# Performance work log

Measured on AMD Instinct MI355X. Metric: run time of the kernel, lower is better.

Reference implementation:

```python
import jax, jax.numpy as jnp
import numpy as np

B, T, IN_DIM, HID_DIM = 64, 1024, 256, 256


def setup_inputs() -> dict:
    key = jax.random.key(0)
    ks = jax.random.split(key, 5)
    glorot = np.sqrt(6.0 / (IN_DIM + HID_DIM * 2)).astype(np.float32)
    def W(k):
        return jax.random.uniform(k, (IN_DIM + HID_DIM, HID_DIM), jnp.float32, -glorot, glorot)
    return {
        "x": jax.random.normal(ks[0], (B, T, IN_DIM), jnp.float32),
        "W_i": W(ks[1]), "b_i": jnp.zeros((HID_DIM,), jnp.float32),
        "W_f": W(ks[2]), "b_f": jnp.zeros((HID_DIM,), jnp.float32),
        "W_o": W(ks[3]), "b_o": jnp.zeros((HID_DIM,), jnp.float32),
        "W_c": W(ks[4]), "b_c": jnp.zeros((HID_DIM,), jnp.float32),
    }


def reference(x, W_i, b_i, W_f, b_f, W_o, b_o, W_c, b_c):
    # x: [B, T, in_dim] -> time-major [T, B, in_dim]
    xt = jnp.transpose(x, (1, 0, 2))
    batch = x.shape[0]
    c0 = jnp.zeros((batch, HID_DIM), x.dtype)
    h0 = jnp.zeros((batch, HID_DIM), x.dtype)

    def step(carry, x_t):
        c, h = carry
        hx = jnp.concatenate([h, x_t], axis=1)  # [B, hid+in]
        i = jax.nn.sigmoid(hx @ W_i + b_i)
        f = jax.nn.sigmoid(hx @ W_f + b_f)
        o = jax.nn.sigmoid(hx @ W_o + b_o)
        c_new = f * c + i * jnp.tanh(hx @ W_c + b_c)
        h_new = o * jnp.tanh(c_new)
        return (c_new, h_new), h_new

    _, outputs = jax.lax.scan(step, (c0, h0), xt)
    return outputs  # [T, B, hid_dim]
```

## Files before the change

kernel.cpp:

```cpp
#include <hip/hip_runtime.h>
#include <hip/hip_fp16.h>
#include <cstdint>

typedef _Float16 f16x8 __attribute__((ext_vector_type(8)));
typedef float f32x4 __attribute__((ext_vector_type(4)));
typedef int i32x4 __attribute__((ext_vector_type(4)));


#define XG_OFF    0ULL
#define XG_BYTES  134217728ULL
#define AP_OFF    (XG_OFF + XG_BYTES)
#define AP_BYTES  33554432ULL
#define BP_OFF    (AP_OFF + AP_BYTES)
#define BP_BYTES  524288ULL
#define WAP_OFF   (BP_OFF + BP_BYTES)
#define WAP_BYTES 262144ULL
#define BIAS_OFF  (WAP_OFF + WAP_BYTES)

#define GLOROT 0.08838834764831845f
#define CSC    (GLOROT / 16129.0f)
#define CSCI   (-1.44269504f * CSC)
#define CSCC   (2.88539008f * CSC)
#define QINV   (127.0f / GLOROT)

#define EXP2(x) __builtin_amdgcn_exp2f(x)
#define RCP(x)  __builtin_amdgcn_rcpf(x)

__global__ void pack_weights(const float* __restrict__ Wi, const float* __restrict__ Wf,
                             const float* __restrict__ Wo, const float* __restrict__ Wc,
                             const float* __restrict__ bi, const float* __restrict__ bf,
                             const float* __restrict__ bo, const float* __restrict__ bc,
                             int8_t* __restrict__ WAp, __half* __restrict__ Bp,
                             float* __restrict__ bias_eff)
{
    int tidg = blockIdx.x * blockDim.x + threadIdx.x;
    if (tidg < 262144) {
        int i  = tidg & 15;
        int l  = (tidg >> 4) & 63;
        int kt = (tidg >> 10) & 3;
        int M  = tidg >> 12;
        int c  = 16 * M + (l & 15);
        int u  = c >> 2, gi = c & 3;
        int khi = kt * 4 + (l >> 4);
        int us  = 16 * khi + 4 * (i & 3) + (i >> 2);
        const float* W = (gi == 0) ? Wi : (gi == 1) ? Wf : (gi == 2) ? Wo : Wc;
        float q = rintf(W[us * 256 + u] * QINV);
        q = fminf(127.f, fmaxf(-127.f, q));
        WAp[tidg] = (int8_t)(int)q;
    } else if (tidg < 262144 + 262144) {
        int beta = tidg - 262144;
        int i = beta & 7;
        int l = (beta >> 3) & 63;
        int kk = (beta >> 9) & 7;
        int n = beta >> 12;
        int c = n * 16 + (l & 15);
        int u = c >> 2, g = c & 3;
        int k = kk * 32 + (l >> 4) * 8 + i;
        const float* W = (g == 0) ? Wi : (g == 1) ? Wf : (g == 2) ? Wo : Wc;
        Bp[beta] = __float2half(W[(256 + k) * 256 + u]);
    } else if (tidg < 262144 + 262144 + 1024) {
        int c = tidg - 524288;
        int g = c & 3;
        const float* bb = (g == 0) ? bi : (g == 1) ? bf : (g == 2) ? bo : bc;
        bias_eff[c] = bb[c >> 2];
    }
}

__global__ void pack_a(const float* __restrict__ x, __half* __restrict__ Ap)
{
    int t = blockIdx.x * blockDim.x + threadIdx.x;
    int l  = t & 63;
    int kk = (t >> 6) & 7;
    int m  = t >> 9;
    int row = m * 16 + (l & 15);
    int k0  = kk * 32 + (l >> 4) * 8;
    const float* src = x + (size_t)row * 256 + k0;
    f16x8 v;
#pragma unroll
    for (int i = 0; i < 8; ++i) v[i] = (_Float16)src[i];
    *reinterpret_cast<f16x8*>(Ap + (size_t)t * 8) = v;
}

__global__ __launch_bounds__(256) void gemm_xg(const __half* __restrict__ Ap,
                                               const __half* __restrict__ Bp,
                                               const float* __restrict__ bias_eff,
                                               __half* __restrict__ xgh)
{
    int wave = threadIdx.x >> 6;
    int lane = threadIdx.x & 63;
    int mtile = blockIdx.x * 4 + wave;
    int ntbase = blockIdx.y * 16;

    f16x8 a[8];
#pragma unroll
    for (int kk = 0; kk < 8; ++kk)
        a[kk] = *reinterpret_cast<const f16x8*>(Ap + ((size_t)(mtile * 8 + kk) * 64 + lane) * 8);

    int col_lo = lane & 15;
    int rgrp = lane >> 4;
#pragma unroll 1
    for (int j = 0; j < 16; ++j) {
        int nt = ntbase + j;
        int c = nt * 16 + col_lo;
        float bb = bias_eff[c];
        f32x4 acc = {bb, bb, bb, bb};
#pragma unroll
        for (int kk = 0; kk < 8; ++kk) {
            f16x8 bfr = *reinterpret_cast<const f16x8*>(Bp + ((size_t)(nt * 8 + kk) * 64 + lane) * 8);
            acc = __builtin_amdgcn_mfma_f32_16x16x32_f16(a[kk], bfr, acc, 0, 0, 0);
        }
        int u = c >> 2, gi = c & 3;
        float gsc = (gi == 3) ? 2.88539008f : -1.44269504f;
        int M2 = u >> 2, rga = u & 3;
        int wv = M2 >> 2, mt = M2 & 3;
#pragma unroll
        for (int r2 = 0; r2 < 4; ++r2) {
            int row = mtile * 16 + rgrp * 4 + r2;
            int b = row >> 10, t = row & 1023;
            int gW = b >> 4, bl = b & 15;
            size_t idx = ((((size_t)(t * 4 + gW) * 16 + wv) * 64 + (rga * 16 + bl)) * 4 + mt) * 4 + gi;
            xgh[idx] = __float2half(acc[r2] * gsc);
        }
    }
}

#define WKL(F) F(0,0) F(0,1) F(0,2) F(0,3) F(1,0) F(1,1) F(1,2) F(1,3) \
  F(2,0) F(2,1) F(2,2) F(2,3) F(3,0) F(3,1) F(3,2) F(3,3)

__global__ __launch_bounds__(1024, 4) void lstm_rec(
    const int8_t* __restrict__ WAp,
    const __half* __restrict__ xgp,
    float* __restrict__ out)
{
    const int g = blockIdx.x;
    const int tid = threadIdx.x;
    const int w = tid >> 6;
    const int l = tid & 63;
    const int bl = l & 15;
    const int rg = l >> 4;

    __shared__ int8_t HB[2][4096];

    const i32x4* wap = reinterpret_cast<const i32x4*>(WAp);
#define DECLW(mt, kt) i32x4 wq_##mt##_##kt = wap[(((4 * w + (mt)) * 4 + (kt)) * 64) + l];
    WKL(DECLW)
#undef DECLW

    int ra[4];
#pragma unroll
    for (int kt = 0; kt < 4; ++kt)
        ra[kt] = bl * 256 + ((((kt * 4) + rg) ^ bl) & 15) * 16;
    const int wab = bl * 256 + ((w ^ bl) & 15) * 16 + rg * 4;

    i32x4 b0 = {0, 0, 0, 0}, b1 = b0, b2 = b0, b3 = b0;
    float cs_0 = 0.f, cs_1 = 0.f, cs_2 = 0.f, cs_3 = 0.f;

    const __half* xp = xgp + ((size_t)(g * 16 + w) * 64 + l) * 16;
    f16x8 xA0 = *reinterpret_cast<const f16x8*>(xp);
    f16x8 xA1 = *reinterpret_cast<const f16x8*>(xp + 8);
    f16x8 xB0, xB1;

    float* op = out + (size_t)(16 * g + bl) * 256 + 16 * w + rg;

#define DOMT(mt, XH) { \
        i32x4 acc = {0, 0, 0, 0}; \
        acc = __builtin_amdgcn_mfma_i32_16x16x64_i8(wq_##mt##_0, b0, acc, 0, 0, 0); \
        acc = __builtin_amdgcn_mfma_i32_16x16x64_i8(wq_##mt##_1, b1, acc, 0, 0, 0); \
        acc = __builtin_amdgcn_mfma_i32_16x16x64_i8(wq_##mt##_2, b2, acc, 0, 0, 0); \
        acc = __builtin_amdgcn_mfma_i32_16x16x64_i8(wq_##mt##_3, b3, acc, 0, 0, 0); \
        float pi = fmaf((float)acc[0], CSCI, (float)XH[(mt) * 4 + 0]); \
        float pf = fmaf((float)acc[1], CSCI, (float)XH[(mt) * 4 + 1]); \
        float po = fmaf((float)acc[2], CSCI, (float)XH[(mt) * 4 + 2]); \
        float pc = fminf(fmaf((float)acc[3], CSCC, (float)XH[(mt) * 4 + 3]), 60.f); \
        float Ei = EXP2(pi), Ef = EXP2(pf), Eo = EXP2(po), Ec = EXP2(pc); \
        float ic = (Ec - 1.f) * RCP((1.f + Ei) * (Ec + 1.f)); \
        float fgt = RCP(1.f + Ef); \
        cs_##mt = fmaf(fgt, cs_##mt, ic); \
        float Fm = EXP2(fminf(2.88539008f * cs_##mt, 60.f)); \
        float hv = (Fm - 1.f) * RCP((1.f + Eo) * (Fm + 1.f)); \
        op[4 * (mt)] = hv; \
        float qm = fmaf(hv, 127.f, 12582912.f); \
        HBB[wab + (mt)] = (int8_t)(__float_as_uint(qm) & 0xffu); }

#define BODY(XC, XC1, XN, XN1, PAR, TNEXT) { \
        const __half* xq = xp + (size_t)(TNEXT) * 65536; \
        XN  = *reinterpret_cast<const f16x8*>(xq); \
        XN1 = *reinterpret_cast<const f16x8*>(xq + 8); \
        int8_t* HBB = HB[PAR]; \
        union { f16x8 v[2]; __half h[16]; } xu; xu.v[0] = XC; xu.v[1] = XC1; \
        DOMT(0, xu.h) DOMT(1, xu.h) DOMT(2, xu.h) DOMT(3, xu.h) \
        asm volatile("s_waitcnt lgkmcnt(0)\n\ts_barrier" ::: "memory"); \
        b0 = *reinterpret_cast<const i32x4*>(HBB + ra[0]); \
        b1 = *reinterpret_cast<const i32x4*>(HBB + ra[1]); \
        b2 = *reinterpret_cast<const i32x4*>(HBB + ra[2]); \
        b3 = *reinterpret_cast<const i32x4*>(HBB + ra[3]); \
        op += 16384; }

    for (int t2 = 0; t2 < 512; ++t2) {
        int te = 2 * t2;
        BODY(xA0, xA1, xB0, xB1, 1, te + 1)
        int tn = (te + 2 < 1024) ? (te + 2) : 1023;
        BODY(xB0, xB1, xA0, xA1, 0, tn)
    }
#undef BODY
#undef DOMT
}

extern "C" void kernel_launch(void* const* d_in, const int* in_sizes, int n_in,
                              void* d_out, int out_size, void* d_ws, size_t ws_size,
                              hipStream_t stream)
{
    const float* x  = (const float*)d_in[0];
    const float* Wi = (const float*)d_in[1];
    const float* bi = (const float*)d_in[2];
    const float* Wf = (const float*)d_in[3];
    const float* bf = (const float*)d_in[4];
    const float* Wo = (const float*)d_in[5];
    const float* bo = (const float*)d_in[6];
    const float* Wc = (const float*)d_in[7];
    const float* bc = (const float*)d_in[8];

    char* ws = (char*)d_ws;
    __half*  xgh      = (__half*)(ws + XG_OFF);
    __half*  Ap       = (__half*)(ws + AP_OFF);
    __half*  Bp       = (__half*)(ws + BP_OFF);
    int8_t*  WAp      = (int8_t*)(ws + WAP_OFF);
    float*   bias_eff = (float*)(ws + BIAS_OFF);

    pack_weights<<<2052, 256, 0, stream>>>(Wi, Wf, Wo, Wc, bi, bf, bo, bc, WAp, Bp, bias_eff);
    pack_a<<<8192, 256, 0, stream>>>(x, Ap);
    gemm_xg<<<dim3(1024, 4), 256, 0, stream>>>(Ap, Bp, bias_eff, xgh);
    lstm_rec<<<4, 1024, 0, stream>>>(WAp, xgh, (float*)d_out);
}
```

Before: 2.287 ms.

## Batch MFMAs ahead of gate math, merge reciprocals, pack h-byte LDS store

Restructures the per-step recurrence body so all four MFMA chains are issued before any gate activation math, giving the scheduler independent work to hide MFMA latency. Two reciprocals for the input and forget gates are merged into a single RCP through a shared denominator. The four int8 hidden-state bytes are packed with v_perm into one 32-bit LDS store instead of four byte stores. The global h output writes are moved after the barrier and the next-step LDS reads, taking them off the critical path before synchronisation. The cost is higher register pressure from holding all accumulators and exponentials live, and a slightly different numeric path for the merged reciprocal.

```diff
diff --git a/kernel.cpp b/kernel.cpp
--- a/kernel.cpp
+++ b/kernel.cpp
@@ -153,7 +153,7 @@
     const int wab = bl * 256 + ((w ^ bl) & 15) * 16 + rg * 4;
 
     i32x4 b0 = {0, 0, 0, 0}, b1 = b0, b2 = b0, b3 = b0;
-    float cs_0 = 0.f, cs_1 = 0.f, cs_2 = 0.f, cs_3 = 0.f;
+    float cs[4] = {0.f, 0.f, 0.f, 0.f};
 
     const __half* xp = xgp + ((size_t)(g * 16 + w) * 64 + l) * 16;
     f16x8 xA0 = *reinterpret_cast<const f16x8*>(xp);
@@ -162,25 +162,13 @@
 
     float* op = out + (size_t)(16 * g + bl) * 256 + 16 * w + rg;
 
-#define DOMT(mt, XH) { \
+#define MFMT(mt) { \
         i32x4 acc = {0, 0, 0, 0}; \
         acc = __builtin_amdgcn_mfma_i32_16x16x64_i8(wq_##mt##_0, b0, acc, 0, 0, 0); \
         acc = __builtin_amdgcn_mfma_i32_16x16x64_i8(wq_##mt##_1, b1, acc, 0, 0, 0); \
         acc = __builtin_amdgcn_mfma_i32_16x16x64_i8(wq_##mt##_2, b2, acc, 0, 0, 0); \
         acc = __builtin_amdgcn_mfma_i32_16x16x64_i8(wq_##mt##_3, b3, acc, 0, 0, 0); \
-        float pi = fmaf((float)acc[0], CSCI, (float)XH[(mt) * 4 + 0]); \
-        float pf = fmaf((float)acc[1], CSCI, (float)XH[(mt) * 4 + 1]); \
-        float po = fmaf((float)acc[2], CSCI, (float)XH[(mt) * 4 + 2]); \
-        float pc = fminf(fmaf((float)acc[3], CSCC, (float)XH[(mt) * 4 + 3]), 60.f); \
-        float Ei = EXP2(pi), Ef = EXP2(pf), Eo = EXP2(po), Ec = EXP2(pc); \
-        float ic = (Ec - 1.f) * RCP((1.f + Ei) * (Ec + 1.f)); \
-        float fgt = RCP(1.f + Ef); \
-        cs_##mt = fmaf(fgt, cs_##mt, ic); \
-        float Fm = EXP2(fminf(2.88539008f * cs_##mt, 60.f)); \
-        float hv = (Fm - 1.f) * RCP((1.f + Eo) * (Fm + 1.f)); \
-        op[4 * (mt)] = hv; \
-        float qm = fmaf(hv, 127.f, 12582912.f); \
-        HBB[wab + (mt)] = (int8_t)(__float_as_uint(qm) & 0xffu); }
+        ac[mt] = acc; }
 
 #define BODY(XC, XC1, XN, XN1, PAR, TNEXT) { \
         const __half* xq = xp + (size_t)(TNEXT) * 65536; \
@@ -188,12 +176,45 @@
         XN1 = *reinterpret_cast<const f16x8*>(xq + 8); \
         int8_t* HBB = HB[PAR]; \
         union { f16x8 v[2]; __half h[16]; } xu; xu.v[0] = XC; xu.v[1] = XC1; \
-        DOMT(0, xu.h) DOMT(1, xu.h) DOMT(2, xu.h) DOMT(3, xu.h) \
+        i32x4 ac[4]; \
+        MFMT(0) MFMT(1) MFMT(2) MFMT(3) \
+         \
+        float Ei[4], Ef[4], Eo[4], Ec[4]; \
+        _Pragma("unroll") \
+        for (int mt = 0; mt < 4; ++mt) { \
+            float pi = fmaf((float)ac[mt][0], CSCI, (float)xu.h[mt * 4 + 0]); \
+            float pf = fmaf((float)ac[mt][1], CSCI, (float)xu.h[mt * 4 + 1]); \
+            float po = fmaf((float)ac[mt][2], CSCI, (float)xu.h[mt * 4 + 2]); \
+            float pc = fminf(fmaf((float)ac[mt][3], CSCC, (float)xu.h[mt * 4 + 3]), 60.f); \
+            Ei[mt] = EXP2(pi); Ef[mt] = EXP2(pf); Eo[mt] = EXP2(po); Ec[mt] = EXP2(pc); \
+        } \
+         \
+        uint32_t qm[4]; \
+        float hv[4]; \
+        _Pragma("unroll") \
+        for (int mt = 0; mt < 4; ++mt) { \
+            float D1 = (1.f + Ei[mt]) * (Ec[mt] + 1.f); \
+            float D2 = 1.f + Ef[mt]; \
+            float r  = RCP(D1 * D2); \
+            float ic = (Ec[mt] - 1.f) * D2 * r; \
+            float fg = D1 * r; \
+            cs[mt] = fmaf(fg, cs[mt], ic); \
+            float Fm = EXP2(fminf(2.88539008f * cs[mt], 60.f)); \
+            float h2 = (Fm - 1.f) * RCP((1.f + Eo[mt]) * (Fm + 1.f)); \
+            hv[mt] = h2; \
+            qm[mt] = __float_as_uint(fmaf(h2, 127.f, 12582912.f)); \
+        } \
+        uint32_t p01 = __builtin_amdgcn_perm(qm[1], qm[0], 0x00000400u); \
+        uint32_t p23 = __builtin_amdgcn_perm(qm[3], qm[2], 0x00000400u); \
+        uint32_t pk  = __builtin_amdgcn_perm(p23, p01, 0x05040100u); \
+        *reinterpret_cast<uint32_t*>(HBB + wab) = pk; \
         asm volatile("s_waitcnt lgkmcnt(0)\n\ts_barrier" ::: "memory"); \
         b0 = *reinterpret_cast<const i32x4*>(HBB + ra[0]); \
         b1 = *reinterpret_cast<const i32x4*>(HBB + ra[1]); \
         b2 = *reinterpret_cast<const i32x4*>(HBB + ra[2]); \
         b3 = *reinterpret_cast<const i32x4*>(HBB + ra[3]); \
+         \
+        op[0] = hv[0]; op[4] = hv[1]; op[8] = hv[2]; op[12] = hv[3]; \
         op += 16384; }
 
     for (int t2 = 0; t2 < 512; ++t2) {
@@ -203,7 +224,7 @@
         BODY(xB0, xB1, xA0, xA1, 0, tn)
     }
 #undef BODY
-#undef DOMT
+#undef MFMT
 }
 
 extern "C" void kernel_launch(void* const* d_in, const int* in_sizes, int n_in,
```

Result: slower. 2.510 ms (+9.7%).
